# Performance work log

Hardware: AMD Instinct MI355X
Metric: run time of the kernel (lower is better)

The kernel has to match this reference:

```python
import jax, jax.numpy as jnp
import numpy as np

GROUPS = 2
STRIDE = (1, 1)
PADDING = ((1, 1), (1, 1))
DILATION = (1, 1)


def setup_inputs() -> dict:
    key = jax.random.key(0)
    k1, k2, k3 = jax.random.split(key, 3)
    B, Cin, H, W = 16, 256, 112, 112
    Cout, kH, kW = 256, 3, 3
    x = jax.random.normal(k1, (B, Cin, H, W), dtype=jnp.float32)
    # kaiming_uniform-like scale: fan_in = (Cin/groups)*kH*kW
    fan_in = (Cin // GROUPS) * kH * kW
    bound = float(np.sqrt(1.0 / fan_in))
    weight = jax.random.uniform(k2, (Cout, Cin // GROUPS, kH, kW), dtype=jnp.float32,
                                minval=-bound, maxval=bound)
    bias = jax.random.uniform(k3, (Cout,), dtype=jnp.float32, minval=-bound, maxval=bound)
    return {"x": x, "weight": weight, "bias": bias}


def reference(x, weight, bias):
    # Grouped conv2d: every backend path of SparseGroupedConv2d (sparse triton
    # active-tile kernel, zero-tile skip, dense F.conv2d fallback) computes this
    # exact grouped convolution; the tile machinery only skips zero-energy tiles.
    y = jax.lax.conv_general_dilated(
        x, weight,
        window_strides=STRIDE,
        padding=PADDING,
        rhs_dilation=DILATION,
        dimension_numbers=("NCHW", "OIHW", "NCHW"),
        feature_group_count=GROUPS,
    )
    return y + bias[None, :, None, None]
```

## Files before the change

kernel.cpp:

```cpp
#include <hip/hip_runtime.h>
#include <hip/hip_bf16.h>
#include <stdint.h>

#define BATCH 16
#define CIN   256
#define HH    112
#define WW    112
#define GROUPS 2
#define CG    128
#define COG   128
#define CK    32
#define NCHUNK 4

typedef __bf16 bf16x8 __attribute__((ext_vector_type(8)));
typedef float  f32x4  __attribute__((ext_vector_type(4)));

#define WB_BYTES   (GROUPS*3*3*COG*CG*2)
#define ZBUF_OFF   WB_BYTES
#define ZBUF_BYTES 8192
#define XB_OFF     (ZBUF_OFF + ZBUF_BYTES)
#define XB_BYTES   ((size_t)BATCH*HH*WW*CIN*2)
#define WS_NEED    ((size_t)XB_OFF + XB_BYTES)

__device__ inline void load_lds16(const void* g, void* l) {
    __builtin_amdgcn_global_load_lds(
        (const __attribute__((address_space(1))) void*)g,
        (__attribute__((address_space(3))) void*)l, 16, 0, 0);
}

__global__ __launch_bounds__(256) void k_wcvt(const float* __restrict__ w,
                                              ushort* __restrict__ wb) {
    int i = blockIdx.x * 256 + threadIdx.x;
    int ci = i & 127;
    int t  = i >> 7;
    int co = t & 127;
    t >>= 7;
    int kw = t % 3; t /= 3;
    int kh = t % 3;
    int g  = t / 3;
    int src = (((g*COG + co)*CG + ci)*3 + kh)*3 + kw;
    __hip_bfloat16 v = __float2bfloat16(w[src]);
    wb[i] = *reinterpret_cast<ushort*>(&v);
}

#define XPAD 113
__global__ __launch_bounds__(256) void k_xcvt(const float* __restrict__ x,
                                              ushort* __restrict__ xb) {
    __shared__ float tile[64 * XPAD];
    int bid = blockIdx.x;
    int cc  = bid & 3;
    int h   = (bid >> 2) % HH;
    int b   = bid / (4 * HH);
    int tid = threadIdx.x;

    const float* src = x + ((size_t)(b*CIN + cc*64) * HH + h) * WW;
    for (int tt = tid; tt < 64*28; tt += 256) {
        int c = tt / 28, v = tt % 28;
        float4 f = *reinterpret_cast<const float4*>(src + (size_t)c*HH*WW + v*4);
        float* d = &tile[c*XPAD + v*4];
        d[0]=f.x; d[1]=f.y; d[2]=f.z; d[3]=f.w;
    }
    __syncthreads();

    if (tid < 224) {
        int w = tid >> 1, half = tid & 1;
        ushort o[32];
#pragma unroll
        for (int j = 0; j < 32; ++j) {
            __hip_bfloat16 v = __float2bfloat16(tile[(half*32 + j)*XPAD + w]);
            o[j] = *reinterpret_cast<ushort*>(&v);
        }
        ushort* dst = xb + (((size_t)(b*HH + h)*WW + w)*CIN + cc*64 + half*32);
        const uint4* o4 = reinterpret_cast<const uint4*>(o);
        uint4* d4 = reinterpret_cast<uint4*>(dst);
        d4[0]=o4[0]; d4[1]=o4[1]; d4[2]=o4[2]; d4[3]=o4[3];
    }
}

__device__ inline void stage_w_all(const ushort* __restrict__ wb, ushort* dstbuf,
                                   int g, int cin, int wave, int lane) {
    int co = wave*16 + (lane >> 2);
    int ts = (lane & 3) ^ ((lane >> 3) & 3);
#pragma unroll
    for (int tap = 0; tap < 9; ++tap) {
        const ushort* src = wb + (((size_t)(g*9 + tap)*COG + co)*CG + cin + ts*8);
        load_lds16(src, dstbuf + (tap*COG + wave*16)*CK);
    }
}

__device__ inline void stage_x(const ushort* __restrict__ xb, ushort* dst,
                               const ushort* __restrict__ zbuf,
                               int b, int g, int oh0, int cin, int wave, int lane) {
    int qv = lane >> 2;
    for (int t = wave; t < 42; t += 8) {
        int rr = t / 7, ii = t % 7;
        int h    = oh0 - 1 + rr;
        int w_in = ii*16 + qv;
        int ts   = (lane & 3) ^ (((2*rr + 1 + qv) >> 1) & 3);
        const ushort* src = (h >= 0 && h < HH)
            ? xb + (((size_t)(b*HH + h)*WW + w_in)*CIN + g*CG + cin + ts*8)
            : zbuf + lane*8;
        load_lds16(src, dst + (rr*114 + 1 + ii*16)*CK);
    }
}

#define XL(XN, KH2, KW2)                                                    \
  {                                                                         \
    int sB_ = lk ^ (((2*(wr + (KH2)) + l15 + (KW2)) >> 1) & 3);             \
    const ushort* bb_ = xcur + ((wr + (KH2))*114 + l15 + (KW2))*CK + sB_*8; \
    _Pragma("unroll")                                                       \
    for (int n_ = 0; n_ < 7; ++n_)                                          \
      XN[n_] = *reinterpret_cast<const bf16x8*>(bb_ + n_*16*CK);            \
  }

#define WL(TAP2)                                                            \
  {                                                                         \
    const ushort* ab_ = wsb + ((TAP2)*COG + wm*64 + l15)*CK + sA*8;         \
    _Pragma("unroll")                                                       \
    for (int u_ = 0; u_ < 4; ++u_)                                          \
      wf[u_] = *reinterpret_cast<const bf16x8*>(ab_ + u_*16*CK);            \
  }

#define MF(XC)                                                              \
    __builtin_amdgcn_s_setprio(1);                                          \
    _Pragma("unroll")                                                       \
    for (int u_ = 0; u_ < 4; ++u_)                                          \
      _Pragma("unroll")                                                     \
      for (int i_ = 0; i_ < 7; ++i_)                                        \
        acc[i_][u_] = __builtin_amdgcn_mfma_f32_16x16x32_bf16(              \
            XC[i_], wf[u_], acc[i_][u_], 0, 0, 0);                          \
    __builtin_amdgcn_s_setprio(0);

__global__ __launch_bounds__(512, 2) void k_conv(const ushort* __restrict__ xb,
                                                 const ushort* __restrict__ wb,
                                                 const float* __restrict__ bias,
                                                 float* __restrict__ out,
                                                 const ushort* __restrict__ zbuf) {
    __shared__ __align__(16) ushort xs[2][6*114*CK];
    __shared__ __align__(16) ushort wsb[9*COG*CK];

    int orig = (blockIdx.x & 7) * 112 + (blockIdx.x >> 3);
    int g   = orig / 448;
    int r   = orig % 448;
    int b   = r / 28;
    int q   = r % 28;
    int oh0 = q * 4;

    int tid  = threadIdx.x;
    int wave = tid >> 6;
    int lane = tid & 63;
    int wm   = wave >> 2;
    int wr   = wave & 3;
    int l15  = lane & 15;
    int lk   = lane >> 4;
    int sA   = lk ^ ((l15 >> 1) & 3);

    for (int t = tid; t < 768; t += 512) {
        int buf = t / 384, r2 = t % 384;
        int rr = r2 / 64, wc = (r2 >> 5) & 1, ch = r2 & 31;
        xs[buf][(rr*114 + wc*113)*CK + ch] = 0;
    }

    float bvreg[4];
#pragma unroll
    for (int u = 0; u < 4; ++u)
        bvreg[u] = bias[g*COG + wm*64 + u*16 + l15];

    f32x4 acc[7][4];
#pragma unroll
    for (int i = 0; i < 7; ++i)
#pragma unroll
        for (int u = 0; u < 4; ++u) acc[i][u] = f32x4{0.f,0.f,0.f,0.f};

    bf16x8 xfA[7], xfB[7], wf[4];

    stage_x(xb, xs[0], zbuf, b, g, oh0, 0, wave, lane);
    stage_w_all(wb, wsb, g, 0, wave, lane);
    __syncthreads();

#pragma unroll 1
    for (int c = 0; c < NCHUNK; ++c) {
        const ushort* xcur = xs[c & 1];
        if (c + 1 < NCHUNK)
            stage_x(xb, xs[(c + 1) & 1], zbuf, b, g, oh0, (c + 1)*CK, wave, lane);

        XL(xfA, 0, 0)
        XL(xfB, 0, 1)  WL(0)  MF(xfA)
        XL(xfA, 0, 2)  WL(1)  MF(xfB)
        XL(xfB, 1, 0)  WL(2)  MF(xfA)
        XL(xfA, 1, 1)  WL(3)  MF(xfB)
        XL(xfB, 1, 2)  WL(4)  MF(xfA)
        XL(xfA, 2, 0)  WL(5)  MF(xfB)
        XL(xfB, 2, 1)  WL(6)  MF(xfA)
        XL(xfA, 2, 2)  WL(7)  MF(xfB)
                       WL(8)  MF(xfA)

        __builtin_amdgcn_sched_barrier(0);
        asm volatile("s_waitcnt lgkmcnt(0)" ::: "memory");
        __builtin_amdgcn_s_barrier();

        if (c + 1 < NCHUNK)
            stage_w_all(wb, wsb, g, (c + 1)*CK, wave, lane);

        __syncthreads();
    }

    int oh = oh0 + wr;
#pragma unroll
    for (int u = 0; u < 4; ++u) {
        int co = g*COG + wm*64 + u*16 + l15;
        float bv = bvreg[u];
        float* obase = out + (((size_t)(b*CIN + co)*HH + oh)*WW + lk*4);
#pragma unroll
        for (int i = 0; i < 7; ++i) {
            f32x4 v;
            v[0] = acc[i][u][0] + bv;
            v[1] = acc[i][u][1] + bv;
            v[2] = acc[i][u][2] + bv;
            v[3] = acc[i][u][3] + bv;
            *reinterpret_cast<f32x4*>(obase + i*16) = v;
        }
    }
}

__global__ __launch_bounds__(128) void k_direct(const float* __restrict__ x,
                                                const float* __restrict__ w,
                                                const float* __restrict__ bias,
                                                float* __restrict__ out) {
    int bid = blockIdx.x;
    int oh  = bid % HH;
    int t   = bid / HH;
    int co  = t % CIN;
    int b   = t / CIN;
    int ow  = threadIdx.x;
    if (ow >= WW) return;
    int g = co / COG;
    float s = bias[co];
    const float* wp = w + (size_t)co*CG*9;
    const float* xp = x + ((size_t)b*CIN + g*CG)*HH*WW;
    for (int ci = 0; ci < CG; ++ci) {
        const float* xr = xp + (size_t)ci*HH*WW;
        const float* wr_ = wp + ci*9;
#pragma unroll
        for (int kh = 0; kh < 3; ++kh) {
            int ih = oh + kh - 1;
            if (ih < 0 || ih >= HH) continue;
#pragma unroll
            for (int kw = 0; kw < 3; ++kw) {
                int iw = ow + kw - 1;
                if (iw < 0 || iw >= WW) continue;
                s += xr[ih*WW + iw] * wr_[kh*3 + kw];
            }
        }
    }
    out[(((size_t)b*CIN + co)*HH + oh)*WW + ow] = s;
}

extern "C" void kernel_launch(void* const* d_in, const int* in_sizes, int n_in,
                              void* d_out, int out_size, void* d_ws, size_t ws_size,
                              hipStream_t stream) {
    const float* x    = (const float*)d_in[0];
    const float* w    = (const float*)d_in[1];
    const float* bias = (const float*)d_in[2];
    float* out        = (float*)d_out;

    if (ws_size >= WS_NEED) {
        ushort* wb   = (ushort*)d_ws;
        ushort* zb   = (ushort*)((char*)d_ws + ZBUF_OFF);
        ushort* xbuf = (ushort*)((char*)d_ws + XB_OFF);
        hipMemsetAsync(zb, 0, ZBUF_BYTES, stream);
        k_wcvt<<<1152, 256, 0, stream>>>(w, wb);
        k_xcvt<<<BATCH*HH*4, 256, 0, stream>>>(x, xbuf);
        k_conv<<<896, 512, 0, stream>>>(xbuf, wb, bias, out, zb);
    } else {
        k_direct<<<BATCH*CIN*HH, 128, 0, stream>>>(x, w, bias, out);
    }
}
```

Measured before the change: 243.0 us.

## Load conv weights directly from global into registers, drop LDS weight staging

The weight conversion kernel now writes weights pre-swizzled in MFMA fragment order. The conv kernel reads each tap's weight fragments straight from global/L2 into registers, double-buffered one tap ahead, instead of staging all nine taps in LDS each chunk. This removes the weight LDS buffer, the per-chunk weight staging and one of the two block barriers per chunk. Input staging now issues a fixed number of LDS-direct loads per wave, padding with dummy loads, so vmcnt-based waits can overlap the next chunk's input loads with compute. In exchange, every wave re-reads weights from cache. The barrier is also placed before the vmcnt wait, which risks a cross-wave race on the freshly loaded input tile.

Measured after the change: 241.3 us. No clear change (-0.7%).

```diff
diff --git a/kernel.cpp b/kernel.cpp
--- a/kernel.cpp
+++ b/kernel.cpp
@@ -31,14 +31,18 @@
 __global__ __launch_bounds__(256) void k_wcvt(const float* __restrict__ w,
                                               ushort* __restrict__ wb) {
     int i = blockIdx.x * 256 + threadIdx.x;
-    int ci = i & 127;
-    int t  = i >> 7;
-    int co = t & 127;
-    t >>= 7;
-    int kw = t % 3; t /= 3;
-    int kh = t % 3;
-    int g  = t / 3;
-    int src = (((g*COG + co)*CG + ci)*3 + kh)*3 + kw;
+    int c8  = i & 7;
+    int l15 = (i >> 3) & 15;
+    int lk  = (i >> 7) & 3;
+    int u   = (i >> 9) & 3;
+    int wm  = (i >> 11) & 1;
+    int hi  = i >> 12;
+    int tap = hi % 9;
+    int gch = hi / 9;
+    int chunk = gch & 3, g = gch >> 2;
+    int co = wm*64 + u*16 + l15;
+    int ci = chunk*32 + lk*8 + c8;
+    int src = ((g*COG + co)*CG + ci)*9 + tap;
     __hip_bfloat16 v = __float2bfloat16(w[src]);
     wb[i] = *reinterpret_cast<ushort*>(&v);
 }
@@ -77,59 +81,55 @@
     }
 }
 
-__device__ inline void stage_w_all(const ushort* __restrict__ wb, ushort* dstbuf,
-                                   int g, int cin, int wave, int lane) {
-    int co = wave*16 + (lane >> 2);
-    int ts = (lane & 3) ^ ((lane >> 3) & 3);
-#pragma unroll
-    for (int tap = 0; tap < 9; ++tap) {
-        const ushort* src = wb + (((size_t)(g*9 + tap)*COG + co)*CG + cin + ts*8);
-        load_lds16(src, dstbuf + (tap*COG + wave*16)*CK);
-    }
-}
-
-__device__ inline void stage_x(const ushort* __restrict__ xb, ushort* dst,
-                               const ushort* __restrict__ zbuf,
-                               int b, int g, int oh0, int cin, int wave, int lane) {
-    int qv = lane >> 2;
-    for (int t = wave; t < 42; t += 8) {
+__device__ inline void xpre48(const ushort* __restrict__ xb, ushort* dstbuf,
+                              ushort* dump, const ushort* __restrict__ zbuf,
+                              int b, int g, int oh0, int cin, int t, int lane) {
+    if (t < 42) {
         int rr = t / 7, ii = t % 7;
-        int h    = oh0 - 1 + rr;
+        int h  = oh0 - 1 + rr;
+        int qv = lane >> 2;
         int w_in = ii*16 + qv;
-        int ts   = (lane & 3) ^ (((2*rr + 1 + qv) >> 1) & 3);
+        int ts = (lane & 3) ^ (((2*rr + 1 + qv) >> 1) & 3);
         const ushort* src = (h >= 0 && h < HH)
             ? xb + (((size_t)(b*HH + h)*WW + w_in)*CIN + g*CG + cin + ts*8)
             : zbuf + lane*8;
-        load_lds16(src, dst + (rr*114 + 1 + ii*16)*CK);
-    }
-}
-
-#define XL(XN, KH2, KW2)                                                    \
+        load_lds16(src, dstbuf + (rr*114 + 1 + ii*16)*CK);
+    } else {
+        load_lds16(zbuf + lane*8, dump);
+    }
+}
+
+#define XLB(BUF, XN, KH2, KW2)                                              \
   {                                                                         \
     int sB_ = lk ^ (((2*(wr + (KH2)) + l15 + (KW2)) >> 1) & 3);             \
-    const ushort* bb_ = xcur + ((wr + (KH2))*114 + l15 + (KW2))*CK + sB_*8; \
+    const ushort* bb_ = (BUF) + ((wr + (KH2))*114 + l15 + (KW2))*CK + sB_*8;\
     _Pragma("unroll")                                                       \
     for (int n_ = 0; n_ < 7; ++n_)                                          \
       XN[n_] = *reinterpret_cast<const bf16x8*>(bb_ + n_*16*CK);            \
   }
 
-#define WL(TAP2)                                                            \
+#define WLG(WN, CN, TN)                                                     \
   {                                                                         \
-    const ushort* ab_ = wsb + ((TAP2)*COG + wm*64 + l15)*CK + sA*8;         \
+    const ushort* wp_ = wlane + ((size_t)((((g4 + (CN))*9 + (TN))*2 + wm)) << 11); \
     _Pragma("unroll")                                                       \
     for (int u_ = 0; u_ < 4; ++u_)                                          \
-      wf[u_] = *reinterpret_cast<const bf16x8*>(ab_ + u_*16*CK);            \
+      WN[u_] = *reinterpret_cast<const bf16x8*>(wp_ + (u_ << 9));           \
   }
 
 #define MF(XC)                                                              \
+    __builtin_amdgcn_sched_barrier(0);                                      \
     __builtin_amdgcn_s_setprio(1);                                          \
     _Pragma("unroll")                                                       \
     for (int u_ = 0; u_ < 4; ++u_)                                          \
       _Pragma("unroll")                                                     \
       for (int i_ = 0; i_ < 7; ++i_)                                        \
         acc[i_][u_] = __builtin_amdgcn_mfma_f32_16x16x32_bf16(              \
-            XC[i_], wf[u_], acc[i_][u_], 0, 0, 0);                          \
+            XC[i_], wfC[u_], acc[i_][u_], 0, 0, 0);                         \
     __builtin_amdgcn_s_setprio(0);
+
+#define ROT4                                                                \
+    _Pragma("unroll")                                                       \
+    for (int u_ = 0; u_ < 4; ++u_) wfC[u_] = wfN[u_];
 
 __global__ __launch_bounds__(512, 2) void k_conv(const ushort* __restrict__ xb,
                                                  const ushort* __restrict__ wb,
@@ -137,7 +137,7 @@
                                                  float* __restrict__ out,
                                                  const ushort* __restrict__ zbuf) {
     __shared__ __align__(16) ushort xs[2][6*114*CK];
-    __shared__ __align__(16) ushort wsb[9*COG*CK];
+    __shared__ __align__(16) ushort dump[512];
 
     int orig = (blockIdx.x & 7) * 112 + (blockIdx.x >> 3);
     int g   = orig / 448;
@@ -153,7 +153,8 @@
     int wr   = wave & 3;
     int l15  = lane & 15;
     int lk   = lane >> 4;
-    int sA   = lk ^ ((l15 >> 1) & 3);
+    int g4   = g * 4;
+    const ushort* wlane = wb + lane*8;
 
     for (int t = tid; t < 768; t += 512) {
         int buf = t / 384, r2 = t % 384;
@@ -161,55 +162,53 @@
         xs[buf][(rr*114 + wc*113)*CK + ch] = 0;
     }
 
-    float bvreg[4];
-#pragma unroll
-    for (int u = 0; u < 4; ++u)
-        bvreg[u] = bias[g*COG + wm*64 + u*16 + l15];
-
     f32x4 acc[7][4];
 #pragma unroll
     for (int i = 0; i < 7; ++i)
 #pragma unroll
         for (int u = 0; u < 4; ++u) acc[i][u] = f32x4{0.f,0.f,0.f,0.f};
 
-    bf16x8 xfA[7], xfB[7], wf[4];
-
-    stage_x(xb, xs[0], zbuf, b, g, oh0, 0, wave, lane);
-    stage_w_all(wb, wsb, g, 0, wave, lane);
-    __syncthreads();
+    bf16x8 xfA[7], xfB[7], wfC[4], wfN[4];
+
+    for (int k2 = 0; k2 < 6; ++k2)
+        xpre48(xb, xs[0], dump, zbuf, b, g, oh0, 0, wave + 8*k2, lane);
+    WLG(wfC, 0, 0)
+    asm volatile("s_waitcnt vmcnt(0)" ::: "memory");
+    __builtin_amdgcn_s_barrier();
+    XLB(xs[0], xfA, 0, 0)
 
 #pragma unroll 1
     for (int c = 0; c < NCHUNK; ++c) {
         const ushort* xcur = xs[c & 1];
+        ushort* xnxt = xs[(c + 1) & 1];
         if (c + 1 < NCHUNK)
-            stage_x(xb, xs[(c + 1) & 1], zbuf, b, g, oh0, (c + 1)*CK, wave, lane);
-
-        XL(xfA, 0, 0)
-        XL(xfB, 0, 1)  WL(0)  MF(xfA)
-        XL(xfA, 0, 2)  WL(1)  MF(xfB)
-        XL(xfB, 1, 0)  WL(2)  MF(xfA)
-        XL(xfA, 1, 1)  WL(3)  MF(xfB)
-        XL(xfB, 1, 2)  WL(4)  MF(xfA)
-        XL(xfA, 2, 0)  WL(5)  MF(xfB)
-        XL(xfB, 2, 1)  WL(6)  MF(xfA)
-        XL(xfA, 2, 2)  WL(7)  MF(xfB)
-                       WL(8)  MF(xfA)
-
-        __builtin_amdgcn_sched_barrier(0);
-        asm volatile("s_waitcnt lgkmcnt(0)" ::: "memory");
-        __builtin_amdgcn_s_barrier();
-
-        if (c + 1 < NCHUNK)
-            stage_w_all(wb, wsb, g, (c + 1)*CK, wave, lane);
-
-        __syncthreads();
+            for (int k2 = 0; k2 < 6; ++k2)
+                xpre48(xb, xnxt, dump, zbuf, b, g, oh0, (c + 1)*CK,
+                       wave + 8*k2, lane);
+
+        WLG(wfN, c, 1)      XLB(xcur, xfB, 0, 1)   MF(xfA)  ROT4
+        WLG(wfN, c, 2)      XLB(xcur, xfA, 0, 2)   MF(xfB)  ROT4
+        WLG(wfN, c, 3)      XLB(xcur, xfB, 1, 0)   MF(xfA)  ROT4
+        WLG(wfN, c, 4)      XLB(xcur, xfA, 1, 1)   MF(xfB)  ROT4
+        WLG(wfN, c, 5)      XLB(xcur, xfB, 1, 2)   MF(xfA)  ROT4
+        WLG(wfN, c, 6)      XLB(xcur, xfA, 2, 0)   MF(xfB)  ROT4
+        WLG(wfN, c, 7)      XLB(xcur, xfB, 2, 1)   MF(xfA)  ROT4
+        WLG(wfN, c, 8)      XLB(xcur, xfA, 2, 2)   MF(xfB)  ROT4
+        WLG(wfN, c + 1, 0)                         MF(xfA)  ROT4
+
+        if (c + 1 < NCHUNK) {
+            asm volatile("s_waitcnt lgkmcnt(0)" ::: "memory");
+            __builtin_amdgcn_s_barrier();
+            asm volatile("s_waitcnt vmcnt(4)" ::: "memory");
+            XLB(xnxt, xfA, 0, 0)
+        }
     }
 
     int oh = oh0 + wr;
 #pragma unroll
     for (int u = 0; u < 4; ++u) {
         int co = g*COG + wm*64 + u*16 + l15;
-        float bv = bvreg[u];
+        float bv = bias[co];
         float* obase = out + (((size_t)(b*CIN + co)*HH + oh)*WW + lk*4);
 #pragma unroll
         for (int i = 0; i < 7; ++i) {
```
